# Kernel optimization log

Measured on AMD Instinct MI355X. Metric: run time of the kernel, lower is better.

Reference implementation:

```python
import jax, jax.numpy as jnp
import numpy as np

B, P, N, C = 2, 64, 256, 512
HEADS = 8
HD = C // HEADS
MLP = int(C * 4.0)
EPS = 1e-5


def setup_inputs() -> dict:
    key = jax.random.key(0)
    ks = jax.random.split(key, 16)
    s = 0.02
    return {
        'x': jax.random.normal(ks[0], (B, P, N, C), jnp.float32),
        'mask': jax.random.randint(ks[1], (B, P, 1, N, N), 0, 2, jnp.int32),
        'pos_scores': jax.random.normal(ks[2], (1, 1, HEADS, N, N), jnp.float32),
        'norm1_w': jnp.ones((C,), jnp.float32),
        'norm1_b': jnp.zeros((C,), jnp.float32),
        'qkv_w': jax.random.normal(ks[3], (3 * C, C), jnp.float32) * s,
        'qkv_b': jnp.zeros((3 * C,), jnp.float32),
        'proj_w': jax.random.normal(ks[4], (C, C), jnp.float32) * s,
        'proj_b': jnp.zeros((C,), jnp.float32),
        'norm2_w': jnp.ones((C,), jnp.float32),
        'norm2_b': jnp.zeros((C,), jnp.float32),
        'mlp_w1': jax.random.normal(ks[5], (MLP, C), jnp.float32) * s,
        'mlp_b1': jnp.zeros((MLP,), jnp.float32),
        'mlp_w2': jax.random.normal(ks[6], (C, MLP), jnp.float32) * s,
        'mlp_b2': jnp.zeros((C,), jnp.float32),
    }


def _group_norm(x, w, b):
    # GroupNorm(C, C) on (b p) c n layout == per-(b,p,c) normalization over n.
    mean = jnp.mean(x, axis=2, keepdims=True)            # [B,P,1,C]
    var = jnp.mean(jnp.square(x - mean), axis=2, keepdims=True)
    return (x - mean) * jax.lax.rsqrt(var + EPS) * w + b


def _attention(x, mask, pos_scores, qkv_w, qkv_b, proj_w, proj_b):
    b, p, n, c = x.shape
    qkv = x @ qkv_w.T + qkv_b                              # [B,P,N,3C]
    qkv = qkv.reshape(b, p, n, 3, HEADS, HD)
    q, k, v = qkv[..., 0, :, :], qkv[..., 1, :, :], qkv[..., 2, :, :]
    scale = HD ** -0.5
    scores = jnp.einsum('bpnhd,bpmhd->bphnm', q * scale, k)  # [B,P,H,N,N]
    scores = scores + pos_scores
    scores = jnp.where(mask > 0, scores, jnp.float32(-1e9))
    attn = jax.nn.softmax(scores, axis=-1)
    out = jnp.einsum('bphnm,bpmhd->bpnhd', attn, v).reshape(b, p, n, c)
    return out @ proj_w.T + proj_b


def reference(x, mask, pos_scores, norm1_w, norm1_b, qkv_w, qkv_b, proj_w,
              proj_b, norm2_w, norm2_b, mlp_w1, mlp_b1, mlp_w2, mlp_b2):
    # attention branch
    x_att = _group_norm(x, norm1_w, norm1_b)
    x_att = _attention(x_att, mask, pos_scores, qkv_w, qkv_b, proj_w, proj_b)
    x = x + x_att
    # mlp branch
    x_mlp = _group_norm(x, norm2_w, norm2_b)
    h = jax.nn.gelu(x_mlp @ mlp_w1.T + mlp_b1, approximate=False)
    x_mlp = h @ mlp_w2.T + mlp_b2
    return x + x_mlp
```

## Files before the change

### kernel.cpp

```cpp
#include <hip/hip_runtime.h>
#include <hip/hip_bf16.h>

constexpr int BB = 2, PP = 64, NN = 256, CC = 512, HH = 8, HD = 64, MLPD = 2048;
constexpr int BP = BB * PP;
constexpr int MTOT = BP * NN;
constexpr float EPS = 1e-5f;

typedef __attribute__((ext_vector_type(8))) short short8_t;
typedef __attribute__((ext_vector_type(4))) short short4_t;
typedef __attribute__((ext_vector_type(4))) float f32x4_t;
typedef __attribute__((ext_vector_type(2))) unsigned int uint2_t;

__device__ inline unsigned short f2bf(float f) {
  union { float f; unsigned u; } v; v.f = f;
  unsigned r = v.u + 0x7fffu + ((v.u >> 16) & 1u);
  return (unsigned short)(r >> 16);
}
__device__ inline float bf2f(unsigned short u) {
  union { unsigned u; float f; } v; v.u = ((unsigned)u) << 16;
  return v.f;
}
__device__ inline unsigned int cvt_pk_bf16(float lo, float hi) {
  unsigned int r;
  asm("v_cvt_pk_bf16_f32 %0, %1, %2" : "=v"(r) : "v"(lo), "v"(hi));
  return r;
}

__device__ inline void async_copy16(unsigned short* lds_base, const unsigned short* g) {
  __builtin_amdgcn_global_load_lds((const __attribute__((address_space(1))) unsigned int*)g,
                                   (__attribute__((address_space(3))) unsigned int*)lds_base,
                                   16, 0, 0);
}

__device__ inline float gelu_fast(float v) {
  float vc = fminf(fmaxf(v, -8.f), 8.f);
  float e = __expf(1.5957691216f * vc + 0.071354816f * vc * vc * vc);
  return v * e * __builtin_amdgcn_rcpf(e + 1.f);
}

__global__ void k_f2bf(const float* __restrict__ in, unsigned short* __restrict__ out, int n) {
  int i = blockIdx.x * blockDim.x + threadIdx.x;
  int stride = gridDim.x * blockDim.x;
  for (; i < n; i += stride) out[i] = f2bf(in[i]);
}

__global__ void k_pack_mask(const int* __restrict__ mask, unsigned short* __restrict__ mt) {
  int idx = blockIdx.x * 256 + threadIdx.x;
  int lr = idx & 15;
  int row = (idx >> 4) & 255;
  int bp = idx >> 12;
  const int* mp = mask + ((size_t)bp * NN + row) * NN;
  unsigned v = 0;
#pragma unroll
  for (int f = 0; f < 16; ++f) v |= (unsigned)(mp[f * 16 + lr] > 0) << f;
  mt[idx] = (unsigned short)v;
}

__global__ void k_pack_pos(const float* __restrict__ pos, unsigned short* __restrict__ pt) {
  int idx = blockIdx.x * 256 + threadIdx.x;
  int f = idx & 15;
  int lr = (idx >> 4) & 15;
  int row = (idx >> 8) & 255;
  int h = idx >> 16;
  pt[idx] = f2bf(pos[((size_t)h * NN + row) * NN + f * 16 + lr]);
}

__global__ void k_gn(const float* __restrict__ x, const float* __restrict__ w,
                     const float* __restrict__ b, unsigned short* __restrict__ out) {
  int bp = blockIdx.x >> 1;
  int c = ((blockIdx.x & 1) << 8) + threadIdx.x;
  const float* xp = x + (size_t)bp * NN * CC + c;
  float s = 0.f, sq = 0.f;
  for (int n = 0; n < NN; ++n) { float v = xp[(size_t)n * CC]; s += v; sq += v * v; }
  float mean = s * (1.f / NN);
  float var = sq * (1.f / NN) - mean * mean;
  float rstd = rsqrtf(var + EPS);
  float ww = w[c], bb = b[c];
  unsigned short* op = out + (size_t)bp * NN * CC + c;
  for (int n = 0; n < NN; ++n) {
    float v = xp[(size_t)n * CC];
    op[(size_t)n * CC] = f2bf((v - mean) * rstd * ww + bb);
  }
}

template <int EPI>
__global__ __launch_bounds__(256) void k_gemm(const unsigned short* __restrict__ A,
                                              const unsigned short* __restrict__ Bw,
                                              const float* __restrict__ bias,
                                              const float* __restrict__ resid,
                                              unsigned short* __restrict__ outb,
                                              float* __restrict__ outf,
                                              unsigned short* __restrict__ qb,
                                              unsigned short* __restrict__ kb,
                                              unsigned short* __restrict__ vtb,
                                              int M, int Nn, int K) {
  constexpr bool SW = (EPI != 3);
  constexpr int BM = 128, BN = 128, BK = 64;
  __shared__ unsigned short As[BM * BK];
  __shared__ unsigned short Bs[BN * BK];
  int tid = threadIdx.x;
  int lane = tid & 63, w = tid >> 6;
  int wm = w >> 1, wn = w & 1;
  int m0 = blockIdx.y * BM, n0 = blockIdx.x * BN;
  int rowc = lane >> 3;
  int csrc = (lane & 7) ^ (rowc & 7);
  int lr = lane & 15, lg = lane >> 4;
  f32x4_t acc[4][4] = {};
  for (int k0 = 0; k0 < K; k0 += BK) {
#pragma unroll
    for (int it = 0; it < 4; ++it) {
      int chunk = w * 4 + it;
      int grow = chunk * 8 + rowc;
      async_copy16(&As[chunk * 512], &A[(size_t)(m0 + grow) * K + k0 + csrc * 8]);
      async_copy16(&Bs[chunk * 512], &Bw[(size_t)(n0 + grow) * K + k0 + csrc * 8]);
    }
    __syncthreads();
#pragma unroll
    for (int kk = 0; kk < BK; kk += 32) {
      int kslot = (kk >> 3) + lg;
      short8_t af[4], bfr[4];
#pragma unroll
      for (int i = 0; i < 4; ++i) {
        int r = wm * 64 + i * 16 + lr;
        af[i] = *(const short8_t*)&As[r * 64 + ((kslot ^ (r & 7)) * 8)];
      }
#pragma unroll
      for (int j = 0; j < 4; ++j) {
        int r = wn * 64 + j * 16 + lr;
        bfr[j] = *(const short8_t*)&Bs[r * 64 + ((kslot ^ (r & 7)) * 8)];
      }
#pragma unroll
      for (int i = 0; i < 4; ++i)
#pragma unroll
        for (int j = 0; j < 4; ++j) {
          if (SW)
            acc[i][j] = __builtin_amdgcn_mfma_f32_16x16x32_bf16(bfr[j], af[i], acc[i][j], 0, 0, 0);
          else
            acc[i][j] = __builtin_amdgcn_mfma_f32_16x16x32_bf16(af[i], bfr[j], acc[i][j], 0, 0, 0);
        }
    }
    __syncthreads();
  }
  if (SW) {
#pragma unroll
    for (int i = 0; i < 4; ++i) {
      int m = m0 + wm * 64 + i * 16 + lr;
#pragma unroll
      for (int j = 0; j < 4; ++j) {
        int n0c = n0 + wn * 64 + j * 16 + lg * 4;
        f32x4_t bv = *(const f32x4_t*)&bias[n0c];
        size_t off = (size_t)m * Nn + n0c;
        if (EPI == 1) {
          float g0 = gelu_fast(acc[i][j][0] + bv[0]);
          float g1 = gelu_fast(acc[i][j][1] + bv[1]);
          float g2 = gelu_fast(acc[i][j][2] + bv[2]);
          float g3 = gelu_fast(acc[i][j][3] + bv[3]);
          uint2_t pk;
          pk[0] = cvt_pk_bf16(g0, g1);
          pk[1] = cvt_pk_bf16(g2, g3);
          *(uint2_t*)&outb[off] = pk;
        } else {
          f32x4_t rv = *(const f32x4_t*)&resid[off];
          f32x4_t o;
#pragma unroll
          for (int r2 = 0; r2 < 4; ++r2) o[r2] = rv[r2] + acc[i][j][r2] + bv[r2];
          *(f32x4_t*)&outf[off] = o;
        }
      }
    }
  } else {
#pragma unroll
    for (int i = 0; i < 4; ++i)
#pragma unroll
      for (int j = 0; j < 4; ++j) {
        int col = n0 + wn * 64 + j * 16 + lr;
        float bv = bias[col];
        int row0 = m0 + wm * 64 + i * 16 + lg * 4;
        int which = col >> 9;
        int hh2 = (col >> 6) & 7;
        int d = col & 63;
        int bp_ = row0 >> 8, m = row0 & 255;
        size_t hb = (size_t)(bp_ * HH + hh2);
        if (which == 2) {
          short4_t pk;
#pragma unroll
          for (int r2 = 0; r2 < 4; ++r2) pk[r2] = (short)f2bf(acc[i][j][r2] + bv);
          *(short4_t*)&vtb[(hb * HD + d) * NN + m] = pk;
        } else if (which == 0) {
#pragma unroll
          for (int r2 = 0; r2 < 4; ++r2)
            qb[(hb * NN + m + r2) * HD + d] = f2bf((acc[i][j][r2] + bv) * 0.125f);
        } else {
#pragma unroll
          for (int r2 = 0; r2 < 4; ++r2)
            kb[(hb * NN + m + r2) * HD + d] = f2bf(acc[i][j][r2] + bv);
        }
      }
  }
}

__global__ __launch_bounds__(256, 2) void k_attn4(const unsigned short* __restrict__ qb,
                                                  const unsigned short* __restrict__ kb,
                                                  const unsigned short* __restrict__ vtb,
                                                  const unsigned short* __restrict__ maskT,
                                                  const unsigned short* __restrict__ posT,
                                                  unsigned short* __restrict__ attn_out) {
  constexpr int LMD = NN + 8;
  __shared__ unsigned short ps[128 * LMD];
  int qt = blockIdx.x, h = blockIdx.y, bp = blockIdx.z;
  int tid = threadIdx.x, lane = tid & 63, w = tid >> 6;
  int lr = lane & 15, lg = lane >> 4;
  int q0w = qt * 128 + w * 32;
  size_t bh = (size_t)(bp * HH + h);
  const unsigned short* Q = qb + bh * NN * HD;
  const unsigned short* K = kb + bh * NN * HD;
  const unsigned short* VT = vtb + bh * HD * NN;
  short8_t qf0[2], qf1[2];
#pragma unroll
  for (int c = 0; c < 2; ++c) {
    qf0[c] = *(const short8_t*)&Q[(size_t)(q0w + c * 16 + lr) * HD + lg * 8];
    qf1[c] = *(const short8_t*)&Q[(size_t)(q0w + c * 16 + lr) * HD + 32 + lg * 8];
  }
  unsigned mbits[2][4];
  short8_t pv0[2][4], pv1[2][4];
#pragma unroll
  for (int c = 0; c < 2; ++c)
#pragma unroll
    for (int r2 = 0; r2 < 4; ++r2) {
      int qrow = q0w + c * 16 + lg * 4 + r2;
      mbits[c][r2] = maskT[((size_t)bp * NN + qrow) * 16 + lr];
      const unsigned short* pp = &posT[(((size_t)h * NN + qrow) * 16 + lr) * 16];
      pv0[c][r2] = *(const short8_t*)&pp[0];
      pv1[c][r2] = *(const short8_t*)&pp[8];
    }
  f32x4_t sc[2][16] = {};
#pragma unroll
  for (int f = 0; f < 16; ++f) {
    short8_t b0 = *(const short8_t*)&K[(size_t)(f * 16 + lr) * HD + lg * 8];
    short8_t b1 = *(const short8_t*)&K[(size_t)(f * 16 + lr) * HD + 32 + lg * 8];
    sc[0][f] = __builtin_amdgcn_mfma_f32_16x16x32_bf16(qf0[0], b0, sc[0][f], 0, 0, 0);
    sc[1][f] = __builtin_amdgcn_mfma_f32_16x16x32_bf16(qf0[1], b0, sc[1][f], 0, 0, 0);
    sc[0][f] = __builtin_amdgcn_mfma_f32_16x16x32_bf16(qf1[0], b1, sc[0][f], 0, 0, 0);
    sc[1][f] = __builtin_amdgcn_mfma_f32_16x16x32_bf16(qf1[1], b1, sc[1][f], 0, 0, 0);
  }
#pragma unroll
  for (int c = 0; c < 2; ++c)
#pragma unroll
    for (int r2 = 0; r2 < 4; ++r2) {
      float mx = -3.0e38f;
#pragma unroll
      for (int f = 0; f < 16; ++f) {
        float pw = bf2f((unsigned short)((f < 8) ? pv0[c][r2][f] : pv1[c][r2][f - 8]));
        float s = ((mbits[c][r2] >> f) & 1) ? (sc[c][f][r2] + pw) : -1.0e9f;
        sc[c][f][r2] = s;
        mx = fmaxf(mx, s);
      }
      for (int d2 = 1; d2 < 16; d2 <<= 1) mx = fmaxf(mx, __shfl_xor(mx, d2));
      float sum = 0.f;
#pragma unroll
      for (int f = 0; f < 16; ++f) { float e = __expf(sc[c][f][r2] - mx); sc[c][f][r2] = e; sum += e; }
      for (int d2 = 1; d2 < 16; d2 <<= 1) sum += __shfl_xor(sum, d2);
      float inv = 1.f / sum;
      int prow = w * 32 + c * 16 + lg * 4 + r2;
#pragma unroll
      for (int f = 0; f < 16; ++f) ps[prow * LMD + f * 16 + lr] = f2bf(sc[c][f][r2] * inv);
    }
  f32x4_t ao[2][4] = {};
#pragma unroll
  for (int kt = 0; kt < 8; ++kt) {
    short8_t a0 = *(const short8_t*)&ps[(w * 32 + lr) * LMD + kt * 32 + lg * 8];
    short8_t a1 = *(const short8_t*)&ps[(w * 32 + 16 + lr) * LMD + kt * 32 + lg * 8];
#pragma unroll
    for (int f = 0; f < 4; ++f) {
      short8_t b = *(const short8_t*)&VT[(size_t)(f * 16 + lr) * NN + kt * 32 + lg * 8];
      ao[0][f] = __builtin_amdgcn_mfma_f32_16x16x32_bf16(a0, b, ao[0][f], 0, 0, 0);
      ao[1][f] = __builtin_amdgcn_mfma_f32_16x16x32_bf16(a1, b, ao[1][f], 0, 0, 0);
    }
  }
#pragma unroll
  for (int c = 0; c < 2; ++c)
#pragma unroll
    for (int f = 0; f < 4; ++f)
#pragma unroll
      for (int r2 = 0; r2 < 4; ++r2) {
        int token = bp * NN + q0w + c * 16 + lg * 4 + r2;
        int d = f * 16 + lr;
        attn_out[(size_t)token * CC + h * HD + d] = f2bf(ao[c][f][r2]);
      }
}

extern "C" void kernel_launch(void* const* d_in, const int* in_sizes, int n_in,
                              void* d_out, int out_size, void* d_ws, size_t ws_size,
                              hipStream_t stream) {
  const float* x      = (const float*)d_in[0];
  const int*   mask   = (const int*)d_in[1];
  const float* pos    = (const float*)d_in[2];
  const float* n1w    = (const float*)d_in[3];
  const float* n1b    = (const float*)d_in[4];
  const float* qkv_w  = (const float*)d_in[5];
  const float* qkv_b  = (const float*)d_in[6];
  const float* proj_w = (const float*)d_in[7];
  const float* proj_b = (const float*)d_in[8];
  const float* n2w    = (const float*)d_in[9];
  const float* n2b    = (const float*)d_in[10];
  const float* w1     = (const float*)d_in[11];
  const float* b1     = (const float*)d_in[12];
  const float* w2     = (const float*)d_in[13];
  const float* b2     = (const float*)d_in[14];
  float* out = (float*)d_out;
  char* ws = (char*)d_ws;

  size_t off = 0;
  auto alloc = [&](size_t bytes) { size_t o = off; off += (bytes + 255) & ~(size_t)255; return o; };
  unsigned short* wqkv  = (unsigned short*)(ws + alloc((size_t)3 * CC * CC * 2));
  unsigned short* wproj = (unsigned short*)(ws + alloc((size_t)CC * CC * 2));
  unsigned short* wm1   = (unsigned short*)(ws + alloc((size_t)MLPD * CC * 2));
  unsigned short* wm2   = (unsigned short*)(ws + alloc((size_t)CC * MLPD * 2));
  unsigned short* maskT = (unsigned short*)(ws + alloc((size_t)BP * NN * 16 * 2));
  unsigned short* posT  = (unsigned short*)(ws + alloc((size_t)HH * NN * NN * 2));
  unsigned short* xn    = (unsigned short*)(ws + alloc((size_t)MTOT * CC * 2));
  float*          x1    = (float*)(ws + alloc((size_t)MTOT * CC * 4));
  size_t region = alloc((size_t)MTOT * MLPD * 2);
  const size_t BUFE = (size_t)MTOT * CC;
  unsigned short* qbuf  = (unsigned short*)(ws + region);
  unsigned short* kbuf  = qbuf + BUFE;
  unsigned short* vtbuf = qbuf + 2 * BUFE;
  unsigned short* attnb = qbuf + 3 * BUFE;
  unsigned short* hbuf  = (unsigned short*)(ws + region);

  k_f2bf<<<1024, 256, 0, stream>>>(qkv_w, wqkv, 3 * CC * CC);
  k_f2bf<<<1024, 256, 0, stream>>>(proj_w, wproj, CC * CC);
  k_f2bf<<<1024, 256, 0, stream>>>(w1, wm1, MLPD * CC);
  k_f2bf<<<1024, 256, 0, stream>>>(w2, wm2, CC * MLPD);
  k_pack_mask<<<2048, 256, 0, stream>>>(mask, maskT);
  k_pack_pos<<<2048, 256, 0, stream>>>(pos, posT);

  k_gn<<<BP * 2, 256, 0, stream>>>(x, n1w, n1b, xn);
  k_gemm<3><<<dim3(3 * CC / 128, MTOT / 128), 256, 0, stream>>>(xn, wqkv, qkv_b, nullptr, nullptr, nullptr, qbuf, kbuf, vtbuf, MTOT, 3 * CC, CC);
  k_attn4<<<dim3(2, HH, BP), 256, 0, stream>>>(qbuf, kbuf, vtbuf, maskT, posT, attnb);
  k_gemm<2><<<dim3(CC / 128, MTOT / 128), 256, 0, stream>>>(attnb, wproj, proj_b, x, nullptr, x1, nullptr, nullptr, nullptr, MTOT, CC, CC);
  k_gn<<<BP * 2, 256, 0, stream>>>(x1, n2w, n2b, xn);
  k_gemm<1><<<dim3(MLPD / 128, MTOT / 128), 256, 0, stream>>>(xn, wm1, b1, nullptr, hbuf, nullptr, nullptr, nullptr, nullptr, MTOT, MLPD, CC);
  k_gemm<2><<<dim3(CC / 128, MTOT / 128), 256, 0, stream>>>(hbuf, wm2, b2, x1, nullptr, out, nullptr, nullptr, nullptr, MTOT, CC, MLPD);
}
```

Baseline: 526.6 us.

## Triple-buffer GEMM LDS tiles and use 8 waves per block

```diff
diff --git a/kernel.cpp b/kernel.cpp
--- a/kernel.cpp
+++ b/kernel.cpp
@@ -84,7 +84,7 @@
 }
 
 template <int EPI>
-__global__ __launch_bounds__(256) void k_gemm(const unsigned short* __restrict__ A,
+__global__ __launch_bounds__(512) void k_gemm(const unsigned short* __restrict__ A,
                                               const unsigned short* __restrict__ Bw,
                                               const float* __restrict__ bias,
                                               const float* __restrict__ resid,
@@ -96,58 +96,82 @@
                                               int M, int Nn, int K) {
   constexpr bool SW = (EPI != 3);
   constexpr int BM = 128, BN = 128, BK = 64;
-  __shared__ unsigned short As[BM * BK];
-  __shared__ unsigned short Bs[BN * BK];
+  __shared__ unsigned short As[3][BM * BK];
+  __shared__ unsigned short Bs[3][BN * BK];
   int tid = threadIdx.x;
   int lane = tid & 63, w = tid >> 6;
-  int wm = w >> 1, wn = w & 1;
+  int wm = w >> 2, wn = w & 3;
   int m0 = blockIdx.y * BM, n0 = blockIdx.x * BN;
   int rowc = lane >> 3;
   int csrc = (lane & 7) ^ (rowc & 7);
   int lr = lane & 15, lg = lane >> 4;
-  f32x4_t acc[4][4] = {};
-  for (int k0 = 0; k0 < K; k0 += BK) {
-#pragma unroll
-    for (int it = 0; it < 4; ++it) {
-      int chunk = w * 4 + it;
+  f32x4_t acc[4][2] = {};
+
+  const int nt = K / BK;
+  auto STAGE = [&](int buf, int t) {
+    int k0 = t * BK;
+#pragma unroll
+    for (int it = 0; it < 2; ++it) {
+      int chunk = w * 2 + it;
       int grow = chunk * 8 + rowc;
-      async_copy16(&As[chunk * 512], &A[(size_t)(m0 + grow) * K + k0 + csrc * 8]);
-      async_copy16(&Bs[chunk * 512], &Bw[(size_t)(n0 + grow) * K + k0 + csrc * 8]);
-    }
-    __syncthreads();
+      async_copy16(&As[buf][chunk * 512], &A[(size_t)(m0 + grow) * K + k0 + csrc * 8]);
+      async_copy16(&Bs[buf][chunk * 512], &Bw[(size_t)(n0 + grow) * K + k0 + csrc * 8]);
+    }
+  };
+  auto COMPUTE = [&](int buf) {
 #pragma unroll
     for (int kk = 0; kk < BK; kk += 32) {
       int kslot = (kk >> 3) + lg;
-      short8_t af[4], bfr[4];
+      short8_t af[4], bfr[2];
 #pragma unroll
       for (int i = 0; i < 4; ++i) {
         int r = wm * 64 + i * 16 + lr;
-        af[i] = *(const short8_t*)&As[r * 64 + ((kslot ^ (r & 7)) * 8)];
-      }
-#pragma unroll
-      for (int j = 0; j < 4; ++j) {
-        int r = wn * 64 + j * 16 + lr;
-        bfr[j] = *(const short8_t*)&Bs[r * 64 + ((kslot ^ (r & 7)) * 8)];
+        af[i] = *(const short8_t*)&As[buf][r * 64 + ((kslot ^ (r & 7)) * 8)];
+      }
+#pragma unroll
+      for (int j = 0; j < 2; ++j) {
+        int r = wn * 32 + j * 16 + lr;
+        bfr[j] = *(const short8_t*)&Bs[buf][r * 64 + ((kslot ^ (r & 7)) * 8)];
       }
 #pragma unroll
       for (int i = 0; i < 4; ++i)
 #pragma unroll
-        for (int j = 0; j < 4; ++j) {
+        for (int j = 0; j < 2; ++j) {
           if (SW)
             acc[i][j] = __builtin_amdgcn_mfma_f32_16x16x32_bf16(bfr[j], af[i], acc[i][j], 0, 0, 0);
           else
             acc[i][j] = __builtin_amdgcn_mfma_f32_16x16x32_bf16(af[i], bfr[j], acc[i][j], 0, 0, 0);
         }
     }
-    __syncthreads();
-  }
+  };
+
+  STAGE(0, 0);
+  STAGE(1, 1);
+  for (int t = 0; t < nt; ++t) {
+    int buf = t - (t / 3) * 3;
+    if (t + 2 < nt) {
+      STAGE((t + 2) - ((t + 2) / 3) * 3, t + 2);
+      asm volatile("s_waitcnt vmcnt(8)" ::: "memory");
+    } else if (t + 2 == nt) {
+      asm volatile("s_waitcnt vmcnt(4)" ::: "memory");
+    } else {
+      asm volatile("s_waitcnt vmcnt(0)" ::: "memory");
+    }
+    __builtin_amdgcn_sched_barrier(0);
+    __builtin_amdgcn_s_barrier();
+    __builtin_amdgcn_sched_barrier(0);
+    COMPUTE(buf);
+    __builtin_amdgcn_sched_barrier(0);
+    __builtin_amdgcn_s_barrier();
+  }
+
   if (SW) {
 #pragma unroll
     for (int i = 0; i < 4; ++i) {
       int m = m0 + wm * 64 + i * 16 + lr;
 #pragma unroll
-      for (int j = 0; j < 4; ++j) {
-        int n0c = n0 + wn * 64 + j * 16 + lg * 4;
+      for (int j = 0; j < 2; ++j) {
+        int n0c = n0 + wn * 32 + j * 16 + lg * 4;
         f32x4_t bv = *(const f32x4_t*)&bias[n0c];
         size_t off = (size_t)m * Nn + n0c;
         if (EPI == 1) {
@@ -172,8 +196,8 @@
 #pragma unroll
     for (int i = 0; i < 4; ++i)
 #pragma unroll
-      for (int j = 0; j < 4; ++j) {
-        int col = n0 + wn * 64 + j * 16 + lr;
+      for (int j = 0; j < 2; ++j) {
+        int col = n0 + wn * 32 + j * 16 + lr;
         float bv = bias[col];
         int row0 = m0 + wm * 64 + i * 16 + lg * 4;
         int which = col >> 9;
@@ -336,10 +360,10 @@
   k_pack_pos<<<2048, 256, 0, stream>>>(pos, posT);
 
   k_gn<<<BP * 2, 256, 0, stream>>>(x, n1w, n1b, xn);
-  k_gemm<3><<<dim3(3 * CC / 128, MTOT / 128), 256, 0, stream>>>(xn, wqkv, qkv_b, nullptr, nullptr, nullptr, qbuf, kbuf, vtbuf, MTOT, 3 * CC, CC);
+  k_gemm<3><<<dim3(3 * CC / 128, MTOT / 128), 512, 0, stream>>>(xn, wqkv, qkv_b, nullptr, nullptr, nullptr, qbuf, kbuf, vtbuf, MTOT, 3 * CC, CC);
   k_attn4<<<dim3(2, HH, BP), 256, 0, stream>>>(qbuf, kbuf, vtbuf, maskT, posT, attnb);
-  k_gemm<2><<<dim3(CC / 128, MTOT / 128), 256, 0, stream>>>(attnb, wproj, proj_b, x, nullptr, x1, nullptr, nullptr, nullptr, MTOT, CC, CC);
+  k_gemm<2><<<dim3(CC / 128, MTOT / 128), 512, 0, stream>>>(attnb, wproj, proj_b, x, nullptr, x1, nullptr, nullptr, nullptr, MTOT, CC, CC);
   k_gn<<<BP * 2, 256, 0, stream>>>(x1, n2w, n2b, xn);
-  k_gemm<1><<<dim3(MLPD / 128, MTOT / 128), 256, 0, stream>>>(xn, wm1, b1, nullptr, hbuf, nullptr, nullptr, nullptr, nullptr, MTOT, MLPD, CC);
-  k_gemm<2><<<dim3(CC / 128, MTOT / 128), 256, 0, stream>>>(hbuf, wm2, b2, x1, nullptr, out, nullptr, nullptr, nullptr, MTOT, CC, MLPD);
-}
+  k_gemm<1><<<dim3(MLPD / 128, MTOT / 128), 512, 0, stream>>>(xn, wm1, b1, nullptr, hbuf, nullptr, nullptr, nullptr, nullptr, MTOT, MLPD, CC);
+  k_gemm<2><<<dim3(CC / 128, MTOT / 128), 512, 0, stream>>>(hbuf, wm2, b2, x1, nullptr, out, nullptr, nullptr, nullptr, MTOT, CC, MLPD);
+}
```

After: 674.4 us. 1.28x slower.
